# Performance work log

Measured on AMD Instinct MI355X. Metric: run time of the kernel, lower is better.

Reference implementation:

```python
import jax, jax.numpy as jnp
import numpy as np

RADIUS = 4
D = 2 * RADIUS + 1  # 9, window diameter


def setup_inputs() -> dict:
    key = jax.random.key(0)
    k1, k2 = jax.random.split(key)
    B, C, H, W = 16, 256, 96, 96
    feat_s = jax.random.normal(k1, (B, C, H, W), dtype=jnp.float32)
    feat_t = jax.random.normal(k2, (B, C, H, W), dtype=jnp.float32)
    return {"feat_s": feat_s, "feat_t": feat_t}


def reference(feat_s, feat_t):
    # feat_s, feat_t: [B, C, H, W]. Output: [B, D*D, H, W] local correlation.
    B, C, H, W = feat_s.shape
    pad = jnp.pad(feat_t, ((0, 0), (0, 0), (RADIUS, RADIUS), (RADIUS, RADIUS)))
    # Loop over the fixed D*D window offsets (81); never materialize the
    # (B, C, D, D, H, W) unfolded tensor. Offset order (dy, dx) row-major
    # matches F.unfold's kernel flattening, so channel index = dy*D + dx.
    corrs = []
    for dy in range(D):
        for dx in range(D):
            win = pad[:, :, dy:dy + H, dx:dx + W]  # [B, C, H, W]
            corrs.append(jnp.einsum('bchw,bchw->bhw', feat_s, win))
    out = jnp.stack(corrs, axis=1) / C  # [B, D*D, H, W]
    return out
```

## Files before the change

kernel.cpp:

```cpp
#include <hip/hip_runtime.h>


#define BB 16
#define CCH 256
#define HH 96
#define WW 96
#define RAD 4
#define DD 9
#define TH 4
#define PP 6
#define CHUNK 4
#define NDYG 3
#define TROWS 6
#define TPAD 104
#define NT 192
#define NTILES (HH/TH)
#define HW (HH*WW)
#define TBUF (CHUNK*TROWS*TPAD)

__global__ __launch_bounds__(NT, 4)
void lcorr2(const float* __restrict__ fs, const float* __restrict__ ft,
            float* __restrict__ out) {
    __shared__ float tl[2][CHUNK][TROWS][TPAD];

    const int g    = blockIdx.x;
    const int dyg  = g % NDYG;
    const int tile = (g / NDYG) % NTILES;
    const int b    = g / (NDYG * NTILES);
    const int h0   = tile * TH;

    const int tid  = threadIdx.x;
    const int wv   = tid >> 6;
    const int lane = tid & 63;
    const int r    = lane >> 4;
    const int wseg = lane & 15;
    const int w0   = wseg * PP;

    for (int i = tid; i < 2 * TBUF; i += NT)
        (&tl[0][0][0][0])[i] = 0.f;

    const float* ftb = ft + (size_t)b * CCH * HW;
    int soff[3]; int loff[3]; bool val[3];
    #pragma unroll
    for (int k = 0; k < 3; ++k) {
        int idx = tid + k * NT;
        int cc  = idx / 144;
        int rem = idx - cc * 144;
        int j   = rem / 24;
        int q   = rem - j * 24;
        int gh  = h0 - RAD + 3 * dyg + j;
        val[k]  = (gh >= 0 && gh < HH);
        soff[k] = cc * HW + (val[k] ? gh : 0) * WW + 4 * q;
        loff[k] = (cc * TROWS + j) * TPAD + 4 + 4 * q;
    }

    const float* sp = fs + (size_t)b * CCH * HW + (h0 + r) * WW + w0;

    float acc[DD][PP];
    #pragma unroll
    for (int i = 0; i < DD; ++i)
        #pragma unroll
        for (int j2 = 0; j2 < PP; ++j2) acc[i][j2] = 0.f;

    const float* ftc = ftb;
    float4 st[3];
    #pragma unroll
    for (int k = 0; k < 3; ++k)
        st[k] = val[k] ? *(const float4*)(ftc + soff[k])
                       : make_float4(0.f, 0.f, 0.f, 0.f);
    __syncthreads();
    #pragma unroll
    for (int k = 0; k < 3; ++k)
        *(float4*)(&tl[0][0][0][0] + loff[k]) = st[k];
    ftc += CHUNK * HW;

    for (int c0 = 0; c0 < CCH; c0 += CHUNK) {
        __syncthreads();
        const int p = (c0 / CHUNK) & 1;
        const bool more = (c0 + CHUNK < CCH);
        if (more) {
            #pragma unroll
            for (int k = 0; k < 3; ++k)
                st[k] = val[k] ? *(const float4*)(ftc + soff[k])
                               : make_float4(0.f, 0.f, 0.f, 0.f);
        }
        #pragma unroll
        for (int cc = 0; cc < CHUNK; ++cc) {
            const float* srow = sp + (size_t)(c0 + cc) * HW;
            float sv[PP];
            #pragma unroll
            for (int u = 0; u < PP / 2; ++u) {
                float2 v = *(const float2*)(srow + 2 * u);
                sv[2 * u] = v.x; sv[2 * u + 1] = v.y;
            }
            const float* trow = &tl[p][cc][r + wv][w0];
            float tv[PP + DD - 1];
            #pragma unroll
            for (int u = 0; u < (PP + DD - 1) / 2; ++u) {
                float2 v = *(const float2*)(trow + 2 * u);
                tv[2 * u] = v.x; tv[2 * u + 1] = v.y;
            }
            #pragma unroll
            for (int dx = 0; dx < DD; ++dx)
                #pragma unroll
                for (int pq = 0; pq < PP; ++pq)
                    acc[dx][pq] = fmaf(sv[pq], tv[pq + dx], acc[dx][pq]);
        }
        if (more) {
            float* dstb = &tl[p ^ 1][0][0][0];
            #pragma unroll
            for (int k = 0; k < 3; ++k)
                *(float4*)(dstb + loff[k]) = st[k];
            ftc += CHUNK * HW;
        }
    }

    const float scale = 1.0f / (float)CCH;
    const int dy = 3 * dyg + wv;
    #pragma unroll
    for (int dx = 0; dx < DD; ++dx) {
        float* op = out + (((size_t)b * (DD * DD) + dy * DD + dx) * HH
                           + (h0 + r)) * WW + w0;
        #pragma unroll
        for (int u = 0; u < PP / 2; ++u) {
            float2 v;
            v.x = acc[dx][2 * u] * scale;
            v.y = acc[dx][2 * u + 1] * scale;
            *(float2*)(op + 2 * u) = v;
        }
    }
}

extern "C" void kernel_launch(void* const* d_in, const int* in_sizes, int n_in,
                              void* d_out, int out_size, void* d_ws, size_t ws_size,
                              hipStream_t stream) {
    const float* fs = (const float*)d_in[0];
    const float* ft = (const float*)d_in[1];
    float* out = (float*)d_out;
    dim3 grid(BB * NTILES * NDYG);
    lcorr2<<<grid, dim3(NT), 0, stream>>>(fs, ft, out);
}
```

Baseline: 434.4 us.

## Pack channel pairs to fp16 and use dot2 accumulation with staged source tile

Converts pairs of channels of both inputs to packed half precision with round-toward-zero conversion as they go into shared memory. The inner loop then uses fdot2, which covers two channels per instruction with fp32 accumulation, roughly halving the math and LDS traffic. The source tile is now also staged through shared memory, and block indices are remapped so each XCD gets a fixed batch for cache locality. Precision drops to fp16 inputs, which risks exceeding tolerance, and the extra LDS buffer and conversion work may lower occupancy.

```diff
diff --git a/kernel.cpp b/kernel.cpp
--- a/kernel.cpp
+++ b/kernel.cpp
@@ -1,5 +1,7 @@
 #include <hip/hip_runtime.h>
 
+
+typedef _Float16 h2 __attribute__((ext_vector_type(2)));
 
 #define BB 16
 #define CCH 256
@@ -9,24 +11,54 @@
 #define DD 9
 #define TH 4
 #define PP 6
-#define CHUNK 4
+#define NPAIR 4
+#define NCHUNK 32
 #define NDYG 3
 #define TROWS 6
 #define TPAD 104
+#define SPAD 96
 #define NT 192
-#define NTILES (HH/TH)
+#define NTILES 24
 #define HW (HH*WW)
-#define TBUF (CHUNK*TROWS*TPAD)
-
-__global__ __launch_bounds__(NT, 4)
-void lcorr2(const float* __restrict__ fs, const float* __restrict__ ft,
+#define TBUF (NPAIR*TROWS*TPAD)
+#define SBUF (NPAIR*TH*SPAD)
+
+static __device__ __forceinline__ h2 bch(unsigned u) {
+    return __builtin_bit_cast(h2, u);
+}
+
+static __device__ __forceinline__ float dot2(unsigned a, unsigned b, float c) {
+#if __has_builtin(__builtin_amdgcn_fdot2)
+    return __builtin_amdgcn_fdot2(bch(a), bch(b), c, false);
+#else
+    h2 x = bch(a), y = bch(b);
+    return fmaf((float)x.x, (float)y.x, fmaf((float)x.y, (float)y.y, c));
+#endif
+}
+
+static __device__ __forceinline__ uint4 pk4(const float4 a, const float4 b) {
+    uint4 r;
+    r.x = __builtin_bit_cast(unsigned, __builtin_amdgcn_cvt_pkrtz(a.x, b.x));
+    r.y = __builtin_bit_cast(unsigned, __builtin_amdgcn_cvt_pkrtz(a.y, b.y));
+    r.z = __builtin_bit_cast(unsigned, __builtin_amdgcn_cvt_pkrtz(a.z, b.z));
+    r.w = __builtin_bit_cast(unsigned, __builtin_amdgcn_cvt_pkrtz(a.w, b.w));
+    return r;
+}
+
+__global__ __launch_bounds__(NT, 3)
+void lcorr3(const float* __restrict__ fs, const float* __restrict__ ft,
             float* __restrict__ out) {
-    __shared__ float tl[2][CHUNK][TROWS][TPAD];
-
-    const int g    = blockIdx.x;
-    const int dyg  = g % NDYG;
-    const int tile = (g / NDYG) % NTILES;
-    const int b    = g / (NDYG * NTILES);
+    __shared__ unsigned tl[2][TBUF];
+    __shared__ unsigned sl[2][SBUF];
+
+    const int x    = blockIdx.x;
+    const int xcd  = x & 7;
+    const int rest = x >> 3;
+    const int bb   = rest & 1;
+    const int td   = rest >> 1;
+    const int b    = xcd + 8 * bb;
+    const int tile = td / NDYG;
+    const int dyg  = td - tile * NDYG;
     const int h0   = tile * TH;
 
     const int tid  = threadIdx.x;
@@ -34,13 +66,12 @@
     const int lane = tid & 63;
     const int r    = lane >> 4;
     const int wseg = lane & 15;
-    const int w0   = wseg * PP;
+    const int w0u  = wseg * PP;
 
     for (int i = tid; i < 2 * TBUF; i += NT)
-        (&tl[0][0][0][0])[i] = 0.f;
-
-    const float* ftb = ft + (size_t)b * CCH * HW;
-    int soff[3]; int loff[3]; bool val[3];
+        (&tl[0][0])[i] = 0u;
+
+    int tsoff[3], tloff[3]; bool tval[3];
     #pragma unroll
     for (int k = 0; k < 3; ++k) {
         int idx = tid + k * NT;
@@ -49,12 +80,24 @@
         int j   = rem / 24;
         int q   = rem - j * 24;
         int gh  = h0 - RAD + 3 * dyg + j;
-        val[k]  = (gh >= 0 && gh < HH);
-        soff[k] = cc * HW + (val[k] ? gh : 0) * WW + 4 * q;
-        loff[k] = (cc * TROWS + j) * TPAD + 4 + 4 * q;
-    }
-
-    const float* sp = fs + (size_t)b * CCH * HW + (h0 + r) * WW + w0;
+        tval[k] = (gh >= 0 && gh < HH);
+        tsoff[k] = 2 * cc * HW + (tval[k] ? gh : 0) * WW + 4 * q;
+        tloff[k] = (cc * TROWS + j) * TPAD + 4 + 4 * q;
+    }
+    int ssoff[2], sloff[2];
+    #pragma unroll
+    for (int k = 0; k < 2; ++k) {
+        int idx = tid + k * NT;
+        int cc  = idx / 96;
+        int rem = idx - cc * 96;
+        int j   = rem / 24;
+        int q   = rem - j * 24;
+        ssoff[k] = 2 * cc * HW + (h0 + j) * WW + 4 * q;
+        sloff[k] = (cc * TH + j) * SPAD + 4 * q;
+    }
+
+    const float* ftc = ft + (size_t)b * CCH * HW;
+    const float* fsc = fs + (size_t)b * CCH * HW;
 
     float acc[DD][PP];
     #pragma unroll
@@ -62,56 +105,81 @@
         #pragma unroll
         for (int j2 = 0; j2 < PP; ++j2) acc[i][j2] = 0.f;
 
-    const float* ftc = ftb;
-    float4 st[3];
-    #pragma unroll
-    for (int k = 0; k < 3; ++k)
-        st[k] = val[k] ? *(const float4*)(ftc + soff[k])
-                       : make_float4(0.f, 0.f, 0.f, 0.f);
-    __syncthreads();
-    #pragma unroll
-    for (int k = 0; k < 3; ++k)
-        *(float4*)(&tl[0][0][0][0] + loff[k]) = st[k];
-    ftc += CHUNK * HW;
-
-    for (int c0 = 0; c0 < CCH; c0 += CHUNK) {
+    {
+        float4 ta[3], tb[3], sa[2], sb[2];
+        #pragma unroll
+        for (int k = 0; k < 3; ++k) {
+            ta[k] = tval[k] ? *(const float4*)(ftc + tsoff[k])
+                            : make_float4(0.f, 0.f, 0.f, 0.f);
+            tb[k] = tval[k] ? *(const float4*)(ftc + tsoff[k] + HW)
+                            : make_float4(0.f, 0.f, 0.f, 0.f);
+        }
+        #pragma unroll
+        for (int k = 0; k < 2; ++k) {
+            sa[k] = *(const float4*)(fsc + ssoff[k]);
+            sb[k] = *(const float4*)(fsc + ssoff[k] + HW);
+        }
         __syncthreads();
-        const int p = (c0 / CHUNK) & 1;
-        const bool more = (c0 + CHUNK < CCH);
+        #pragma unroll
+        for (int k = 0; k < 3; ++k)
+            *(uint4*)(&tl[0][tloff[k]]) = pk4(ta[k], tb[k]);
+        #pragma unroll
+        for (int k = 0; k < 2; ++k)
+            *(uint4*)(&sl[0][sloff[k]]) = pk4(sa[k], sb[k]);
+        ftc += 2 * NPAIR * HW;
+        fsc += 2 * NPAIR * HW;
+    }
+
+    for (int c = 0; c < NCHUNK; ++c) {
+        __syncthreads();
+        const int p = c & 1;
+        const bool more = (c + 1 < NCHUNK);
+        float4 ta[3], tb[3], sa[2], sb[2];
         if (more) {
             #pragma unroll
-            for (int k = 0; k < 3; ++k)
-                st[k] = val[k] ? *(const float4*)(ftc + soff[k])
-                               : make_float4(0.f, 0.f, 0.f, 0.f);
-        }
-        #pragma unroll
-        for (int cc = 0; cc < CHUNK; ++cc) {
-            const float* srow = sp + (size_t)(c0 + cc) * HW;
-            float sv[PP];
+            for (int k = 0; k < 3; ++k) {
+                ta[k] = tval[k] ? *(const float4*)(ftc + tsoff[k])
+                                : make_float4(0.f, 0.f, 0.f, 0.f);
+                tb[k] = tval[k] ? *(const float4*)(ftc + tsoff[k] + HW)
+                                : make_float4(0.f, 0.f, 0.f, 0.f);
+            }
+            #pragma unroll
+            for (int k = 0; k < 2; ++k) {
+                sa[k] = *(const float4*)(fsc + ssoff[k]);
+                sb[k] = *(const float4*)(fsc + ssoff[k] + HW);
+            }
+        }
+        #pragma unroll
+        for (int pp = 0; pp < NPAIR; ++pp) {
+            const unsigned* srow = &sl[p][(pp * TH + r) * SPAD + w0u];
+            unsigned sv[PP];
             #pragma unroll
             for (int u = 0; u < PP / 2; ++u) {
-                float2 v = *(const float2*)(srow + 2 * u);
+                uint2 v = *(const uint2*)(srow + 2 * u);
                 sv[2 * u] = v.x; sv[2 * u + 1] = v.y;
             }
-            const float* trow = &tl[p][cc][r + wv][w0];
-            float tv[PP + DD - 1];
+            const unsigned* trow = &tl[p][(pp * TROWS + r + wv) * TPAD + w0u];
+            unsigned tv[PP + DD - 1];
             #pragma unroll
             for (int u = 0; u < (PP + DD - 1) / 2; ++u) {
-                float2 v = *(const float2*)(trow + 2 * u);
+                uint2 v = *(const uint2*)(trow + 2 * u);
                 tv[2 * u] = v.x; tv[2 * u + 1] = v.y;
             }
             #pragma unroll
             for (int dx = 0; dx < DD; ++dx)
                 #pragma unroll
-                for (int pq = 0; pq < PP; ++pq)
-                    acc[dx][pq] = fmaf(sv[pq], tv[pq + dx], acc[dx][pq]);
+                for (int q = 0; q < PP; ++q)
+                    acc[dx][q] = dot2(sv[q], tv[q + dx], acc[dx][q]);
         }
         if (more) {
-            float* dstb = &tl[p ^ 1][0][0][0];
             #pragma unroll
             for (int k = 0; k < 3; ++k)
-                *(float4*)(dstb + loff[k]) = st[k];
-            ftc += CHUNK * HW;
+                *(uint4*)(&tl[p ^ 1][tloff[k]]) = pk4(ta[k], tb[k]);
+            #pragma unroll
+            for (int k = 0; k < 2; ++k)
+                *(uint4*)(&sl[p ^ 1][sloff[k]]) = pk4(sa[k], sb[k]);
+            ftc += 2 * NPAIR * HW;
+            fsc += 2 * NPAIR * HW;
         }
     }
 
@@ -120,7 +188,7 @@
     #pragma unroll
     for (int dx = 0; dx < DD; ++dx) {
         float* op = out + (((size_t)b * (DD * DD) + dy * DD + dx) * HH
-                           + (h0 + r)) * WW + w0;
+                           + (h0 + r)) * WW + w0u;
         #pragma unroll
         for (int u = 0; u < PP / 2; ++u) {
             float2 v;
@@ -138,5 +206,5 @@
     const float* ft = (const float*)d_in[1];
     float* out = (float*)d_out;
     dim3 grid(BB * NTILES * NDYG);
-    lcorr2<<<grid, dim3(NT), 0, stream>>>(fs, ft, out);
-}
+    lcorr3<<<grid, dim3(NT), 0, stream>>>(fs, ft, out);
+}
```

After: 368.4 us. 1.18x faster.
